# Kernel optimization log

Measured on AMD Instinct MI355X. Metric: run time of the kernel, lower is better.

The kernel has to match this reference:

```python
import jax, jax.numpy as jnp
import numpy as np

N_NODES = 100000
HIDDEN = 128
E = 524288  # edges per graph (pos and neg)


def setup_inputs() -> dict:
    key = jax.random.key(0)
    ks = jax.random.split(key, 8)
    return {
        "z_src": jax.random.normal(ks[0], (N_NODES, HIDDEN), dtype=jnp.float32),
        "z_dst": jax.random.normal(ks[1], (N_NODES, HIDDEN), dtype=jnp.float32),
        "pos_src": jax.random.randint(ks[2], (E,), 0, N_NODES, dtype=jnp.int64),
        "pos_dst": jax.random.randint(ks[3], (E,), 0, N_NODES, dtype=jnp.int64),
        "neg_src": jax.random.randint(ks[4], (E,), 0, N_NODES, dtype=jnp.int64),
        "neg_dst": jax.random.randint(ks[5], (E,), 0, N_NODES, dtype=jnp.int64),
        "W1": jax.random.normal(ks[6], (2 * HIDDEN, HIDDEN), dtype=jnp.float32) * (1.0 / np.sqrt(2 * HIDDEN)),
        "b1": jnp.zeros((HIDDEN,), dtype=jnp.float32),
        "W2": jax.random.normal(ks[7], (HIDDEN, 1), dtype=jnp.float32) * (1.0 / np.sqrt(HIDDEN)),
        "b2": jnp.zeros((1,), dtype=jnp.float32),
    }


def reference(z_src, z_dst, pos_src, pos_dst, neg_src, neg_dst, W1, b1, W2, b2):
    # Gather endpoint features for pos then neg edges (cat along edge dim)
    src_idx = jnp.concatenate([pos_src, neg_src])  # [2E]
    dst_idx = jnp.concatenate([pos_dst, neg_dst])  # [2E]
    z = jnp.concatenate([z_src[src_idx], z_dst[dst_idx]], axis=-1)  # [2E, 2h]
    z = jax.nn.relu(z @ W1 + b1)  # [2E, h]
    z = z @ W2 + b2               # [2E, 1]
    return z.reshape(-1)
```

## Files before the change

kernel.cpp:

```cpp
#include <hip/hip_runtime.h>
#include <hip/hip_bf16.h>
#include <cstdint>

#define N_NODES 100000
#define HIDDEN  128
#define NEDGE   524288
#define NT      6250
#define PBLK    256
#define WSTRIDE (PBLK * 4)

typedef __attribute__((ext_vector_type(8))) short short8;
typedef __attribute__((ext_vector_type(4))) float f32x4;

__device__ __forceinline__ unsigned short f2b(float f) {
    unsigned u = __float_as_uint(f);
    u += 0x7FFFu + ((u >> 16) & 1u);
    return (unsigned short)(u >> 16);
}
__device__ __forceinline__ float b2f(unsigned x16) {
    return __uint_as_float(x16 << 16);
}

__device__ __forceinline__ void async_copy16(const float* g, float* l) {
    __builtin_amdgcn_global_load_lds(
        (const __attribute__((address_space(1))) unsigned int*)g,
        (__attribute__((address_space(3))) unsigned int*)l,
        16, 0, 0);
}

__global__ void wp_kernel(const float* __restrict__ W1,
                          unsigned short* __restrict__ Wp)
{
    const int f = blockIdx.x;
    const int tb = blockIdx.y;
    const int lane = threadIdx.x;
    const int t = lane & 15, q = lane >> 4;
    const int n = f >> 2, ks = f & 3;
    short8 v;
#pragma unroll
    for (int j = 0; j < 8; ++j)
        v[j] = (short)f2b(W1[(size_t)(tb * 128 + ks * 32 + q * 8 + j) * 128 + n * 16 + t]);
    *(short8*)(Wp + ((size_t)(tb * 32 + f) * 64 + lane) * 8) = v;
}

__global__ __launch_bounds__(256, 2)
void precompute_kernel(const float* __restrict__ z_src,
                       const float* __restrict__ z_dst,
                       const unsigned short* __restrict__ Wp,
                       const float* __restrict__ b1,
                       unsigned short* __restrict__ Asrc,
                       unsigned short* __restrict__ Adst)
{
    const int table = blockIdx.y;
    const float* __restrict__ z = table ? z_dst : z_src;
    unsigned short* __restrict__ A = table ? Adst : Asrc;

    __shared__ float zbuf[4][2][2048];

    const int tid = threadIdx.x;
    const int wave = tid >> 6;
    const int lane = tid & 63;
    const int t = lane & 15;
    const int q = lane >> 4;

    short8 wfrag[32];
    {
        const unsigned short* wp = Wp + ((size_t)table * 32 * 64 + lane) * 8;
#pragma unroll
        for (int f = 0; f < 32; ++f)
            wfrag[f] = *(const short8*)(wp + (size_t)f * 64 * 8);
    }

    float4 b1v[8];
#pragma unroll
    for (int n = 0; n < 8; ++n)
        b1v[n] = (table == 0) ? *(const float4*)(b1 + n * 16 + q * 4)
                              : make_float4(0.f, 0.f, 0.f, 0.f);

    const int lhi = lane >> 5;
    const int llo = lane & 31;
#define STAGE(m0, p)                                                          \
    do {                                                                      \
        _Pragma("unroll")                                                     \
        for (int j = 0; j < 8; ++j) {                                         \
            const int r = j * 2 + lhi;                                        \
            const int c = llo ^ (r & 7);                                      \
            async_copy16(z + (size_t)((m0) + r) * 128 + c * 4,                \
                         &zbuf[wave][p][j * 256]);                            \
        }                                                                     \
    } while (0)

    int tile = blockIdx.x * 4 + wave;
    int p = 0;
    STAGE(tile * 16, 0);
    __builtin_amdgcn_s_waitcnt(0xF70);
    asm volatile("" ::: "memory");

    while (tile < NT) {
        const int m0 = tile * 16;
        const int ntile = tile + WSTRIDE;
        const int nm0 = (ntile < NT ? ntile : tile) * 16;
        STAGE(nm0, p ^ 1);
        asm volatile("" ::: "memory");
        __builtin_amdgcn_s_waitcnt(0xF78);
        asm volatile("" ::: "memory");

        short8 b[4];
#pragma unroll
        for (int ks = 0; ks < 4; ++ks) {
            const int c0 = ks * 8 + 2 * q;
            const int s = t & 7;
            const float4 v0 = *(const float4*)&zbuf[wave][p][(t * 32 + (c0 ^ s)) * 4];
            const float4 v1 = *(const float4*)&zbuf[wave][p][(t * 32 + ((c0 + 1) ^ s)) * 4];
            b[ks][0] = (short)f2b(v0.x); b[ks][1] = (short)f2b(v0.y);
            b[ks][2] = (short)f2b(v0.z); b[ks][3] = (short)f2b(v0.w);
            b[ks][4] = (short)f2b(v1.x); b[ks][5] = (short)f2b(v1.y);
            b[ks][6] = (short)f2b(v1.z); b[ks][7] = (short)f2b(v1.w);
        }

        f32x4 acc[8];
#pragma unroll
        for (int n = 0; n < 8; ++n) acc[n] = (f32x4){0.f, 0.f, 0.f, 0.f};
#pragma unroll
        for (int n = 0; n < 8; ++n)
#pragma unroll
            for (int ks = 0; ks < 4; ++ks)
                acc[n] = __builtin_amdgcn_mfma_f32_16x16x32_bf16(
                             wfrag[n * 4 + ks], b[ks], acc[n], 0, 0, 0);

        unsigned short* ob = (unsigned short*)&zbuf[wave][p][0];
        const int sw = (t & 7) * 2;
#pragma unroll
        for (int n = 0; n < 8; ++n) {
            ushort4 h;
            h.x = f2b(acc[n][0] + b1v[n].x);
            h.y = f2b(acc[n][1] + b1v[n].y);
            h.z = f2b(acc[n][2] + b1v[n].z);
            h.w = f2b(acc[n][3] + b1v[n].w);
            *(ushort4*)&ob[t * 136 + (((n * 4 + q) ^ sw) * 4)] = h;
        }
        const int rr = lane >> 4;
#pragma unroll
        for (int it = 0; it < 4; ++it) {
            const int r = it * 4 + rr;
            const uint4 v = *(const uint4*)&ob[r * 136 + (((2 * t) ^ ((r & 7) * 2)) * 4)];
            *(uint4*)(A + (size_t)(m0 + r) * 128 + t * 8) = v;
        }
        asm volatile("" ::: "memory");

        p ^= 1;
        tile = ntile;
    }
#undef STAGE
}

__global__ __launch_bounds__(256, 6)
void edge_kernel(const unsigned short* __restrict__ Asrc,
                 const unsigned short* __restrict__ Adst,
                 const int* __restrict__ pos_src,
                 const int* __restrict__ pos_dst,
                 const int* __restrict__ neg_src,
                 const int* __restrict__ neg_dst,
                 const float* __restrict__ W2,
                 const float* __restrict__ b2,
                 float* __restrict__ out)
{
    const int tid = threadIdx.x;
    const int t = tid & 15;
    const int g = tid >> 4;

    const bool is_pos = blockIdx.x < 4096;
    const int* __restrict__ sp = is_pos ? pos_src : neg_src;
    const int* __restrict__ dp = is_pos ? pos_dst : neg_dst;
    const int eb = (is_pos ? (int)blockIdx.x : (int)blockIdx.x - 4096) * 128;

    float w2r[8];
#pragma unroll
    for (int j = 0; j < 8; ++j) w2r[j] = W2[t * 8 + j];
    const float bias2 = b2[0];

    int sidx[8], didx[8];
#pragma unroll
    for (int i = 0; i < 8; ++i) {
        sidx[i] = sp[eb + i * 16 + g];
        didx[i] = dp[eb + i * 16 + g];
    }

    uint4 ua[2][2], ub[2][2];
#pragma unroll
    for (int k = 0; k < 2; ++k) {
        ua[0][k] = *(const uint4*)(Asrc + (size_t)sidx[k] * 128 + t * 8);
        ub[0][k] = *(const uint4*)(Adst + (size_t)didx[k] * 128 + t * 8);
    }
    asm volatile("" ::: "memory");

#pragma unroll
    for (int c = 0; c < 4; ++c) {
        if (c < 3) {
#pragma unroll
            for (int k = 0; k < 2; ++k) {
                ua[(c + 1) & 1][k] =
                    *(const uint4*)(Asrc + (size_t)sidx[(c + 1) * 2 + k] * 128 + t * 8);
                ub[(c + 1) & 1][k] =
                    *(const uint4*)(Adst + (size_t)didx[(c + 1) * 2 + k] * 128 + t * 8);
            }
        }
        asm volatile("" ::: "memory");
#pragma unroll
        for (int k = 0; k < 2; ++k) {
            const unsigned* pa = (const unsigned*)&ua[c & 1][k];
            const unsigned* pb = (const unsigned*)&ub[c & 1][k];
            float acc = 0.f;
#pragma unroll
            for (int j2 = 0; j2 < 4; ++j2) {
                float h0 = b2f(pa[j2] & 0xFFFFu) + b2f(pb[j2] & 0xFFFFu);
                float h1 = b2f(pa[j2] >> 16)     + b2f(pb[j2] >> 16);
                h0 = fmaxf(h0, 0.f);
                h1 = fmaxf(h1, 0.f);
                acc = fmaf(h0, w2r[2 * j2], acc);
                acc = fmaf(h1, w2r[2 * j2 + 1], acc);
            }
            acc += __shfl_xor(acc, 1);
            acc += __shfl_xor(acc, 2);
            acc += __shfl_xor(acc, 4);
            acc += __shfl_xor(acc, 8);
            if (t == 0) out[blockIdx.x * 128 + (c * 2 + k) * 16 + g] = acc + bias2;
        }
    }
}

extern "C" void kernel_launch(void* const* d_in, const int* in_sizes, int n_in,
                              void* d_out, int out_size, void* d_ws, size_t ws_size,
                              hipStream_t stream) {
    const float* z_src  = (const float*)d_in[0];
    const float* z_dst  = (const float*)d_in[1];
    const int* pos_src  = (const int*)d_in[2];
    const int* pos_dst  = (const int*)d_in[3];
    const int* neg_src  = (const int*)d_in[4];
    const int* neg_dst  = (const int*)d_in[5];
    const float* W1     = (const float*)d_in[6];
    const float* b1     = (const float*)d_in[7];
    const float* W2     = (const float*)d_in[8];
    const float* b2     = (const float*)d_in[9];
    float* out = (float*)d_out;

    unsigned short* Asrc = (unsigned short*)d_ws;
    unsigned short* Adst = Asrc + (size_t)N_NODES * HIDDEN;
    unsigned short* Wp   = Adst + (size_t)N_NODES * HIDDEN;

    wp_kernel<<<dim3(32, 2), 64, 0, stream>>>(W1, Wp);

    precompute_kernel<<<dim3(PBLK, 2), 256, 0, stream>>>(z_src, z_dst, Wp, b1,
                                                         Asrc, Adst);

    edge_kernel<<<8192, 256, 0, stream>>>(Asrc, Adst, pos_src, pos_dst,
                                          neg_src, neg_dst, W2, b2, out);
}
```

Measured before the change: 222.3 us.

## Triple-buffer precompute staging and issue all edge gathers up front

The precompute kernel moves from 4-wave blocks with double-buffered LDS staging to 2-wave blocks with a three-deep ring of async global-to-LDS copies. The grid grows to 384 blocks per table and the waitcnt is adjusted so two tiles stay in flight, hiding more load latency. The edge kernel drops its two-stage software pipeline and issues all 16 row gathers per thread before computing, trading registers (occupancy hint lowered from 6 to 4) for more memory-level parallelism. The 2-wave blocks may leave LDS-limited occupancy lower, and a late block's second prefetch can read rows beyond the table when tile+WSTRIDE reaches NT.

```diff
diff --git a/kernel.cpp b/kernel.cpp
--- a/kernel.cpp
+++ b/kernel.cpp
@@ -6,8 +6,8 @@
 #define HIDDEN  128
 #define NEDGE   524288
 #define NT      6250
-#define PBLK    256
-#define WSTRIDE (PBLK * 4)
+#define PBLK    384
+#define WSTRIDE (PBLK * 2)
 
 typedef __attribute__((ext_vector_type(8))) short short8;
 typedef __attribute__((ext_vector_type(4))) float f32x4;
@@ -43,7 +43,7 @@
     *(short8*)(Wp + ((size_t)(tb * 32 + f) * 64 + lane) * 8) = v;
 }
 
-__global__ __launch_bounds__(256, 2)
+__global__ __launch_bounds__(128, 2)
 void precompute_kernel(const float* __restrict__ z_src,
                        const float* __restrict__ z_dst,
                        const unsigned short* __restrict__ Wp,
@@ -55,7 +55,7 @@
     const float* __restrict__ z = table ? z_dst : z_src;
     unsigned short* __restrict__ A = table ? Adst : Asrc;
 
-    __shared__ float zbuf[4][2][2048];
+    __shared__ float zbuf[2][3][2048];
 
     const int tid = threadIdx.x;
     const int wave = tid >> 6;
@@ -90,19 +90,21 @@
         }                                                                     \
     } while (0)
 
-    int tile = blockIdx.x * 4 + wave;
-    int p = 0;
+    int tile = blockIdx.x * 2 + wave;
     STAGE(tile * 16, 0);
+    STAGE((tile + WSTRIDE) * 16, 1);
     __builtin_amdgcn_s_waitcnt(0xF70);
     asm volatile("" ::: "memory");
 
+    int p = 0;
     while (tile < NT) {
         const int m0 = tile * 16;
-        const int ntile = tile + WSTRIDE;
-        const int nm0 = (ntile < NT ? ntile : tile) * 16;
-        STAGE(nm0, p ^ 1);
+        const int t2 = tile + 2 * WSTRIDE;
+        const int sm0 = (t2 < NT ? t2 : tile) * 16;
+        int ps = p + 2; if (ps >= 3) ps -= 3;
+        STAGE(sm0, ps);
         asm volatile("" ::: "memory");
-        __builtin_amdgcn_s_waitcnt(0xF78);
+        __builtin_amdgcn_s_waitcnt(0x4F70);
         asm volatile("" ::: "memory");
 
         short8 b[4];
@@ -148,13 +150,13 @@
         }
         asm volatile("" ::: "memory");
 
-        p ^= 1;
-        tile = ntile;
+        tile += WSTRIDE;
+        ++p; if (p >= 3) p -= 3;
     }
 #undef STAGE
 }
 
-__global__ __launch_bounds__(256, 6)
+__global__ __launch_bounds__(256, 4)
 void edge_kernel(const unsigned short* __restrict__ Asrc,
                  const unsigned short* __restrict__ Adst,
                  const int* __restrict__ pos_src,
@@ -186,46 +188,32 @@
         didx[i] = dp[eb + i * 16 + g];
     }
 
-    uint4 ua[2][2], ub[2][2];
-#pragma unroll
-    for (int k = 0; k < 2; ++k) {
-        ua[0][k] = *(const uint4*)(Asrc + (size_t)sidx[k] * 128 + t * 8);
-        ub[0][k] = *(const uint4*)(Adst + (size_t)didx[k] * 128 + t * 8);
-    }
-    asm volatile("" ::: "memory");
-
-#pragma unroll
-    for (int c = 0; c < 4; ++c) {
-        if (c < 3) {
-#pragma unroll
-            for (int k = 0; k < 2; ++k) {
-                ua[(c + 1) & 1][k] =
-                    *(const uint4*)(Asrc + (size_t)sidx[(c + 1) * 2 + k] * 128 + t * 8);
-                ub[(c + 1) & 1][k] =
-                    *(const uint4*)(Adst + (size_t)didx[(c + 1) * 2 + k] * 128 + t * 8);
-            }
-        }
-        asm volatile("" ::: "memory");
-#pragma unroll
-        for (int k = 0; k < 2; ++k) {
-            const unsigned* pa = (const unsigned*)&ua[c & 1][k];
-            const unsigned* pb = (const unsigned*)&ub[c & 1][k];
-            float acc = 0.f;
-#pragma unroll
-            for (int j2 = 0; j2 < 4; ++j2) {
-                float h0 = b2f(pa[j2] & 0xFFFFu) + b2f(pb[j2] & 0xFFFFu);
-                float h1 = b2f(pa[j2] >> 16)     + b2f(pb[j2] >> 16);
-                h0 = fmaxf(h0, 0.f);
-                h1 = fmaxf(h1, 0.f);
-                acc = fmaf(h0, w2r[2 * j2], acc);
-                acc = fmaf(h1, w2r[2 * j2 + 1], acc);
-            }
-            acc += __shfl_xor(acc, 1);
-            acc += __shfl_xor(acc, 2);
-            acc += __shfl_xor(acc, 4);
-            acc += __shfl_xor(acc, 8);
-            if (t == 0) out[blockIdx.x * 128 + (c * 2 + k) * 16 + g] = acc + bias2;
-        }
+    uint4 ua[8], ub[8];
+#pragma unroll
+    for (int i = 0; i < 8; ++i) {
+        ua[i] = *(const uint4*)(Asrc + (size_t)sidx[i] * 128 + t * 8);
+        ub[i] = *(const uint4*)(Adst + (size_t)didx[i] * 128 + t * 8);
+    }
+
+#pragma unroll
+    for (int i = 0; i < 8; ++i) {
+        float acc = 0.f;
+        const unsigned* pa = (const unsigned*)&ua[i];
+        const unsigned* pb = (const unsigned*)&ub[i];
+#pragma unroll
+        for (int j2 = 0; j2 < 4; ++j2) {
+            float h0 = b2f(pa[j2] & 0xFFFFu) + b2f(pb[j2] & 0xFFFFu);
+            float h1 = b2f(pa[j2] >> 16)     + b2f(pb[j2] >> 16);
+            h0 = fmaxf(h0, 0.f);
+            h1 = fmaxf(h1, 0.f);
+            acc = fmaf(h0, w2r[2 * j2], acc);
+            acc = fmaf(h1, w2r[2 * j2 + 1], acc);
+        }
+        acc += __shfl_xor(acc, 1);
+        acc += __shfl_xor(acc, 2);
+        acc += __shfl_xor(acc, 4);
+        acc += __shfl_xor(acc, 8);
+        if (t == 0) out[blockIdx.x * 128 + i * 16 + g] = acc + bias2;
     }
 }
 
@@ -250,7 +238,7 @@
 
     wp_kernel<<<dim3(32, 2), 64, 0, stream>>>(W1, Wp);
 
-    precompute_kernel<<<dim3(PBLK, 2), 256, 0, stream>>>(z_src, z_dst, Wp, b1,
+    precompute_kernel<<<dim3(PBLK, 2), 128, 0, stream>>>(z_src, z_dst, Wp, b1,
                                                          Asrc, Adst);
 
     edge_kernel<<<8192, 256, 0, stream>>>(Asrc, Adst, pos_src, pos_dst,
```

Measured after the change: 224.0 us. About the same (+0.8%).
